# Kernel optimization log

Hardware: AMD Instinct MI355X
Metric: run time of the kernel (lower is better)

The kernel has to match this reference:

```python
import jax, jax.numpy as jnp
import numpy as np

TOP_K = 4
N_GROUP = 4
TOPK_GROUP = 2
ROUTED_SCALING = 1.0


def setup_inputs() -> dict:
    key = jax.random.key(0)
    k1, k2, k3, k4, k5 = jax.random.split(key, 5)
    B, S, H, I, E = 1, 2048, 1024, 512, 16
    hidden_states = jax.random.normal(k1, (B, S, H), dtype=jnp.float32)
    # router weight (kaiming-uniform-like scale)
    gate_weight = jax.random.normal(k2, (E, H), dtype=jnp.float32) * (1.0 / np.sqrt(H))
    e_bias = jnp.zeros((E,), dtype=jnp.float32)  # e_score_correction_bias buffer
    gate_proj = jax.random.normal(k3, (E, I, H), dtype=jnp.float32) * 0.02
    up_proj = jax.random.normal(k4, (E, I, H), dtype=jnp.float32) * 0.02
    down_proj = jax.random.normal(k5, (E, H, I), dtype=jnp.float32) * 0.02
    return {
        "hidden_states": hidden_states,
        "gate_weight": gate_weight,
        "e_bias": e_bias,
        "gate_proj": gate_proj,
        "up_proj": up_proj,
        "down_proj": down_proj,
    }


def _route(x_flat, gate_weight, e_bias):
    # x_flat: [T, H]
    T = x_flat.shape[0]
    E = gate_weight.shape[0]
    logits = jnp.einsum("th,eh->te", x_flat, gate_weight)
    scores = jax.nn.sigmoid(logits)                      # [T, E]
    scores_for_choice = scores + e_bias[None, :]
    # group scores = sum of top-2 expert scores within each group
    grp = scores_for_choice.reshape(T, N_GROUP, E // N_GROUP)
    top2, _ = jax.lax.top_k(grp, 2)
    group_scores = top2.sum(axis=-1)                     # [T, G]
    _, group_idx = jax.lax.top_k(group_scores, TOPK_GROUP)
    group_mask = jax.nn.one_hot(group_idx, N_GROUP, dtype=scores.dtype).sum(axis=1)  # [T, G]
    score_mask = jnp.repeat(group_mask, E // N_GROUP, axis=1)                        # [T, E]
    tmp_scores = jnp.where(score_mask > 0, scores_for_choice, 0.0)
    _, topk_idx = jax.lax.top_k(tmp_scores, TOP_K)       # [T, K]
    topk_weight = jnp.take_along_axis(scores, topk_idx, axis=1)
    denom = topk_weight.sum(axis=-1, keepdims=True) + 1e-20
    topk_weight = topk_weight / denom * ROUTED_SCALING
    return topk_idx, topk_weight


def reference(hidden_states, gate_weight, e_bias, gate_proj, up_proj, down_proj):
    B, S, H = hidden_states.shape
    E = gate_proj.shape[0]
    x = hidden_states.reshape(-1, H).astype(jnp.float32)  # [T, H]
    topk_idx, topk_weight = _route(x, gate_weight, e_bias)
    # combine weights per (token, expert): sum over the k slots selecting e
    combine = (jax.nn.one_hot(topk_idx, E, dtype=x.dtype) * topk_weight[..., None]).sum(axis=1)  # [T, E]
    # dense expert MLP (mathematically equal to gather-compute-scatter since
    # non-selected experts receive zero combine weight)
    g = jnp.einsum("th,eih->tei", x, gate_proj)
    u = jnp.einsum("th,eih->tei", x, up_proj)
    act = jax.nn.silu(g) * u                              # [T, E, I]
    expert_out = jnp.einsum("tei,ehi->teh", act, down_proj)
    y = jnp.einsum("teh,te->th", expert_out, combine)
    return y.reshape(B, S, H)
```

## Files before the change

kernel.cpp:

```cpp
#include <hip/hip_runtime.h>
#include <hip/hip_bf16.h>

typedef __attribute__((ext_vector_type(8))) short bf16x8;
typedef __attribute__((ext_vector_type(4))) float f32x4;

#define T_TOK 2048
#define HD 1024
#define ID 512
#define NE 16
#define TOPK 4
#define BK 32
#define WELEM (HD*ID*NE)
#define CPAD 16

__device__ __forceinline__ unsigned pk2(float a, float b) {
    return __builtin_amdgcn_perm(__float_as_uint(b), __float_as_uint(a),
                                 0x07060302u);
}
__device__ __forceinline__ bf16x8 cvt8(const float* __restrict__ p) {
    float4 a = *(const float4*)p;
    float4 b = *(const float4*)(p + 4);
    union { bf16x8 v; unsigned u[4]; } r;
    r.u[0] = pk2(a.x, a.y); r.u[1] = pk2(a.z, a.w);
    r.u[2] = pk2(b.x, b.y); r.u[3] = pk2(b.z, b.w);
    return r.v;
}
__device__ __forceinline__ short f2bf(float f) {
    unsigned u = __float_as_uint(f);
    return (short)((u + 0x7fffu + ((u >> 16) & 1u)) >> 16);
}
__device__ __forceinline__ float bf2f(short s) {
    return __uint_as_float(((unsigned)(unsigned short)s) << 16);
}
__device__ __forceinline__ void load_lds16(const short* g, short* l) {
    __builtin_amdgcn_global_load_lds(
        (const __attribute__((address_space(1))) unsigned*)g,
        (__attribute__((address_space(3))) unsigned*)l, 16, 0, 0);
}

#define MFMA_BF16 __builtin_amdgcn_mfma_f32_16x16x32_bf16

__global__ __launch_bounds__(256) void conv_k(
        const float* __restrict__ s0, short* __restrict__ d0,
        const float* __restrict__ s1, short* __restrict__ d1,
        const float* __restrict__ s2, short* __restrict__ d2,
        int* __restrict__ counts) {
    if (blockIdx.x == 0 && blockIdx.y == 0)
        counts[threadIdx.x] = 0;
    const float* src = (blockIdx.y == 0) ? s0 : (blockIdx.y == 1) ? s1 : s2;
    short* dst       = (blockIdx.y == 0) ? d0 : (blockIdx.y == 1) ? d1 : d2;
    size_t i = ((size_t)blockIdx.x * 256 + threadIdx.x) * 8;
    union { bf16x8 v; uint4 q; } r;
    r.v = cvt8(src + i);
    *(uint4*)(dst + i) = r.q;
}

__global__ __launch_bounds__(256) void router_k(
        const float* __restrict__ x, const float* __restrict__ gw,
        const float* __restrict__ eb,
        int* __restrict__ tk_idx, float* __restrict__ tk_w,
        short* __restrict__ xb,
        int* __restrict__ counts, int* __restrict__ tok_list,
        int* __restrict__ pair_slot) {
    int wid  = (blockIdx.x * 256 + threadIdx.x) >> 6;
    int lane = threadIdx.x & 63;

    const float* xr = x + (size_t)wid * HD + lane * 16;
    float xv[16];
#pragma unroll
    for (int c = 0; c < 4; c++) {
        float4 v = *(const float4*)(xr + c * 4);
        xv[4 * c] = v.x; xv[4 * c + 1] = v.y; xv[4 * c + 2] = v.z; xv[4 * c + 3] = v.w;
    }
    {
        union { uint4 q; unsigned u[4]; } w0, w1;
        w0.u[0] = pk2(xv[0], xv[1]);  w0.u[1] = pk2(xv[2], xv[3]);
        w0.u[2] = pk2(xv[4], xv[5]);  w0.u[3] = pk2(xv[6], xv[7]);
        w1.u[0] = pk2(xv[8], xv[9]);  w1.u[1] = pk2(xv[10], xv[11]);
        w1.u[2] = pk2(xv[12], xv[13]); w1.u[3] = pk2(xv[14], xv[15]);
        short* d = xb + ((size_t)wid << 10) + lane * 16;
        *(uint4*)d = w0.q;
        *(uint4*)(d + 8) = w1.q;
    }

    float logits[NE];
#pragma unroll
    for (int e = 0; e < NE; e++) {
        const float* gr = gw + e * HD + lane * 16;
        float p = 0.f;
#pragma unroll
        for (int c = 0; c < 4; c++) {
            float4 v = *(const float4*)(gr + c * 4);
            p += xv[4 * c] * v.x + xv[4 * c + 1] * v.y +
                 xv[4 * c + 2] * v.z + xv[4 * c + 3] * v.w;
        }
#pragma unroll
        for (int s = 32; s > 0; s >>= 1) p += __shfl_xor(p, s, 64);
        logits[e] = p;
    }

    float scores[NE], sc[NE];
#pragma unroll
    for (int e = 0; e < NE; e++) {
        scores[e] = 1.f / (1.f + __expf(-logits[e]));
        sc[e] = scores[e] + eb[e];
    }

    float gs[4];
#pragma unroll
    for (int g = 0; g < 4; g++) {
        float a = sc[4 * g], b = sc[4 * g + 1], c = sc[4 * g + 2], d = sc[4 * g + 3];
        float h1 = fmaxf(a, b), l1 = fminf(a, b);
        float h2 = fmaxf(c, d), l2 = fminf(c, d);
        gs[g] = fmaxf(h1, h2) + fmaxf(fminf(h1, h2), fmaxf(l1, l2));
    }
    int g0 = 0; float b0 = gs[0];
#pragma unroll
    for (int g = 1; g < 4; g++) if (gs[g] > b0) { b0 = gs[g]; g0 = g; }
    int g1 = -1; float b1 = -1e30f;
#pragma unroll
    for (int g = 0; g < 4; g++) if (g != g0 && gs[g] > b1) { b1 = gs[g]; g1 = g; }

    int taken = 0;
    int bid[TOPK]; float bsc[TOPK]; float wsum = 0.f;
#pragma unroll
    for (int k = 0; k < TOPK; k++) {
        float bv = -1e30f; int bi = 0; float bs = 0.f;
#pragma unroll
        for (int e = 0; e < NE; e++) {
            int grp = e >> 2;
            bool ok = ((grp == g0) || (grp == g1)) && !((taken >> e) & 1);
            if (ok && sc[e] > bv) { bv = sc[e]; bi = e; bs = scores[e]; }
        }
        taken |= (1 << bi);
        bid[k] = bi; bsc[k] = bs; wsum += bs;
    }
    if (lane < TOPK) {
        float inv = 1.0f / (wsum + 1e-20f);
        int ee = bid[lane];
        int slot = atomicAdd(&counts[ee * CPAD], 1);
        tok_list[ee * T_TOK + slot] = wid;
        pair_slot[wid * TOPK + lane] = slot;
        tk_idx[wid * TOPK + lane] = ee;
        tk_w[wid * TOPK + lane]   = bsc[lane] * inv;
    }
}

__global__ __launch_bounds__(256) void gemm1_k(
        const short* __restrict__ xb,
        const short* __restrict__ gpb,
        const short* __restrict__ upb,
        const int* __restrict__ counts,
        const int* __restrict__ tok_list,
        short* __restrict__ act) {
    __shared__ short xs[3][128 * BK];
    __shared__ short gs[3][64 * BK];
    __shared__ short us[3][64 * BK];
    __shared__ int   tok_s[128];

    int e = blockIdx.x;
    int cnt = counts[e * CPAD];
    int base = blockIdx.z * 128;
    if (base >= cnt) return;
    int off = 0;
#pragma unroll
    for (int q = 0; q < NE; q++) if (q < e) off += counts[q * CPAD];
    int arow0 = off + base;

    int tid = threadIdx.x;
    if (tid < 128) {
        int s = base + tid;
        tok_s[tid] = (s < cnt) ? tok_list[e * T_TOK + s] : tok_list[e * T_TOK];
    }
    __syncthreads();

    int wv = tid >> 6, lane = tid & 63;
    int qd = lane >> 4, l16 = lane & 15;
    int wm = (wv >> 1) * 64, wn = (wv & 1) * 32;
    int nb0 = blockIdx.y * 64;
    const short* gp = gpb + (size_t)e * ID * HD + (size_t)nb0 * HD;
    const short* up = upb + (size_t)e * ID * HD + (size_t)nb0 * HD;

    const short* xsg[2]; short* xld[2];
#pragma unroll
    for (int i = 0; i < 2; i++) {
        int idx = i * 256 + tid, r = idx >> 2, c = idx & 3;
        int f = (r >> 1) & 3;
        xsg[i] = xb + ((size_t)tok_s[r] << 10) + ((c ^ f) << 3);
        xld[i] = &xs[0][(i * 256 + wv * 64) * 8];
    }
    const short* gsg; const short* usg; short* gld; short* uld;
    {
        int r = tid >> 2, c = tid & 3;
        int f = (r >> 1) & 3;
        size_t so = (size_t)r * HD + ((c ^ f) << 3);
        gsg = gp + so;
        usg = up + so;
        gld = &gs[0][(wv * 64) * 8];
        uld = &us[0][(wv * 64) * 8];
    }

    f32x4 accg[4][2] = {};
    f32x4 accu[4][2] = {};

    auto STAGE = [&](int kp, int b) {
        load_lds16(xsg[0] + kp, xld[0] + b * (128 * BK));
        load_lds16(xsg[1] + kp, xld[1] + b * (128 * BK));
        load_lds16(gsg + kp, gld + b * (64 * BK));
        load_lds16(usg + kp, uld + b * (64 * BK));
    };
    auto COMPUTE = [&](int b) {
        const short* xsb = xs[b];
        const short* gsb = gs[b];
        const short* usb = us[b];
        bf16x8 af[4], bg[2], bu[2];
#pragma unroll
        for (int i = 0; i < 4; i++) {
            int r = wm + i * 16 + l16;
            af[i] = *(const bf16x8*)&xsb[r * BK + ((qd ^ ((r >> 1) & 3)) << 3)];
        }
#pragma unroll
        for (int j = 0; j < 2; j++) {
            int r = wn + j * 16 + l16;
            int lo = r * BK + ((qd ^ ((r >> 1) & 3)) << 3);
            bg[j] = *(const bf16x8*)&gsb[lo];
            bu[j] = *(const bf16x8*)&usb[lo];
        }
#pragma unroll
        for (int i = 0; i < 4; i++)
#pragma unroll
            for (int j = 0; j < 2; j++) {
                accg[i][j] = MFMA_BF16(af[i], bg[j], accg[i][j], 0, 0, 0);
                accu[i][j] = MFMA_BF16(af[i], bu[j], accu[i][j], 0, 0, 0);
            }
    };

    constexpr int NP = HD / BK;
    STAGE(0, 0); STAGE(BK, 1);
    int b = 0;
#pragma unroll 1
    for (int p = 0; p < NP; ++p) {
        int bn = b + 2; if (bn >= 3) bn -= 3;
        if (p + 2 < NP) {
            STAGE((p + 2) * BK, bn);
            asm volatile("s_waitcnt vmcnt(8)" ::: "memory");
        } else if (p + 1 < NP) {
            asm volatile("s_waitcnt vmcnt(4)" ::: "memory");
        } else {
            asm volatile("s_waitcnt vmcnt(0)" ::: "memory");
        }
        __builtin_amdgcn_s_barrier();
        asm volatile("" ::: "memory");
        COMPUTE(b);
        asm volatile("" ::: "memory");
        __builtin_amdgcn_s_barrier();
        b = (b == 2) ? 0 : b + 1;
    }

#pragma unroll
    for (int i = 0; i < 4; i++)
#pragma unroll
        for (int j = 0; j < 2; j++)
#pragma unroll
            for (int r = 0; r < 4; r++) {
                int m = wm + i * 16 + qd * 4 + r;
                if (base + m < cnt) {
                    float g = accg[i][j][r], u = accu[i][j][r];
                    float a = g / (1.f + __expf(-g)) * u;
                    act[(size_t)(arow0 + m) * ID + nb0 + wn + j * 16 + l16] = f2bf(a);
                }
            }
}

__global__ __launch_bounds__(256) void gemm2_k(
        const short* __restrict__ act,
        const short* __restrict__ dpb,
        const int* __restrict__ counts,
        short* __restrict__ yexp) {
    __shared__ short as_[3][128 * BK];
    __shared__ short ds_[3][128 * BK];

    int e = blockIdx.x;
    int cnt = counts[e * CPAD];
    int base = blockIdx.z * 128;
    if (base >= cnt) return;
    int off = 0;
#pragma unroll
    for (int q = 0; q < NE; q++) if (q < e) off += counts[q * CPAD];
    int arow0 = off + base;

    int tid = threadIdx.x;
    int wv = tid >> 6, lane = tid & 63;
    int qd = lane >> 4, l16 = lane & 15;
    int wm = (wv >> 1) * 64, wn = (wv & 1) * 64;
    int hb0 = blockIdx.y * 128;
    const short* dp = dpb + (size_t)e * HD * ID + (size_t)hb0 * ID;

    const short* asg[2]; const short* dsg[2]; short* ald[2]; short* dld[2];
#pragma unroll
    for (int i = 0; i < 2; i++) {
        int idx = i * 256 + tid, r = idx >> 2, c = idx & 3;
        int f = (r >> 1) & 3;
        int sw = (c ^ f) << 3;
        asg[i] = act + (size_t)(arow0 + r) * ID + sw;
        dsg[i] = dp + (size_t)r * ID + sw;
        ald[i] = &as_[0][(i * 256 + wv * 64) * 8];
        dld[i] = &ds_[0][(i * 256 + wv * 64) * 8];
    }

    f32x4 acc[4][4] = {};

    auto STAGE = [&](int kp, int b) {
        load_lds16(asg[0] + kp, ald[0] + b * (128 * BK));
        load_lds16(asg[1] + kp, ald[1] + b * (128 * BK));
        load_lds16(dsg[0] + kp, dld[0] + b * (128 * BK));
        load_lds16(dsg[1] + kp, dld[1] + b * (128 * BK));
    };
    auto COMPUTE = [&](int b) {
        const short* asb = as_[b];
        const short* dsb = ds_[b];
        bf16x8 af[4], bd[4];
#pragma unroll
        for (int i = 0; i < 4; i++) {
            int r = wm + i * 16 + l16;
            af[i] = *(const bf16x8*)&asb[r * BK + ((qd ^ ((r >> 1) & 3)) << 3)];
            int r2 = wn + i * 16 + l16;
            bd[i] = *(const bf16x8*)&dsb[r2 * BK + ((qd ^ ((r2 >> 1) & 3)) << 3)];
        }
#pragma unroll
        for (int i = 0; i < 4; i++)
#pragma unroll
            for (int j = 0; j < 4; j++)
                acc[i][j] = MFMA_BF16(af[i], bd[j], acc[i][j], 0, 0, 0);
    };

    constexpr int NP = ID / BK;
    STAGE(0, 0); STAGE(BK, 1);
    int b = 0;
#pragma unroll 1
    for (int p = 0; p < NP; ++p) {
        int bn = b + 2; if (bn >= 3) bn -= 3;
        if (p + 2 < NP) {
            STAGE((p + 2) * BK, bn);
            asm volatile("s_waitcnt vmcnt(8)" ::: "memory");
        } else if (p + 1 < NP) {
            asm volatile("s_waitcnt vmcnt(4)" ::: "memory");
        } else {
            asm volatile("s_waitcnt vmcnt(0)" ::: "memory");
        }
        __builtin_amdgcn_s_barrier();
        asm volatile("" ::: "memory");
        COMPUTE(b);
        asm volatile("" ::: "memory");
        __builtin_amdgcn_s_barrier();
        b = (b == 2) ? 0 : b + 1;
    }

#pragma unroll
    for (int i = 0; i < 4; i++)
#pragma unroll
        for (int j = 0; j < 4; j++)
#pragma unroll
            for (int r = 0; r < 4; r++) {
                int m = wm + i * 16 + qd * 4 + r;
                if (base + m < cnt)
                    yexp[(size_t)(arow0 + m) * HD + hb0 + wn + j * 16 + l16] =
                        f2bf(acc[i][j][r]);
            }
}

__global__ __launch_bounds__(256) void combine_k(
        const short* __restrict__ yexp,
        const int* __restrict__ counts,
        const int* __restrict__ tk_idx, const float* __restrict__ tk_w,
        const int* __restrict__ pair_slot,
        float* __restrict__ out) {
    __shared__ int offs_s[NE];
    if (threadIdx.x == 0) {
        int a = 0;
#pragma unroll
        for (int e = 0; e < NE; e++) { offs_s[e] = a; a += counts[e * CPAD]; }
    }
    __syncthreads();

    int t = blockIdx.x * 2 + (threadIdx.x >> 7);
    int i = threadIdx.x & 127;
    float acc[8] = {};
#pragma unroll
    for (int k = 0; k < TOPK; k++) {
        int p = t * TOPK + k;
        int e = tk_idx[p];
        int row = offs_s[e] + pair_slot[p];
        float w = tk_w[p];
        bf16x8 v = *(const bf16x8*)(yexp + (size_t)row * HD + i * 8);
#pragma unroll
        for (int j = 0; j < 8; j++) acc[j] += w * bf2f(v[j]);
    }
    float4 o0 = {acc[0], acc[1], acc[2], acc[3]};
    float4 o1 = {acc[4], acc[5], acc[6], acc[7]};
    float* d = out + (size_t)t * HD + i * 8;
    *(float4*)d = o0;
    *(float4*)(d + 4) = o1;
}

extern "C" void kernel_launch(void* const* d_in, const int* in_sizes, int n_in,
                              void* d_out, int out_size, void* d_ws, size_t ws_size,
                              hipStream_t stream) {
    const float* x  = (const float*)d_in[0];
    const float* gw = (const float*)d_in[1];
    const float* eb = (const float*)d_in[2];
    const float* gp = (const float*)d_in[3];
    const float* up = (const float*)d_in[4];
    const float* dp = (const float*)d_in[5];

    short* gpb = (short*)d_ws;
    short* upb = gpb + WELEM;
    short* dpb = upb + WELEM;
    short* xb  = dpb + WELEM;
    short* act = xb + (size_t)T_TOK * HD;
    int* counts    = (int*)(act + (size_t)(T_TOK * TOPK + 128) * ID);
    int* tok_list  = counts + NE * CPAD;
    int* pair_slot = tok_list + NE * T_TOK;
    int* tk_idx    = pair_slot + T_TOK * TOPK;
    float* tk_w    = (float*)(tk_idx + T_TOK * TOPK);
    short* yexp = gpb;

    conv_k<<<dim3(WELEM / 8 / 256, 3), 256, 0, stream>>>(gp, gpb, up, upb,
                                                         dp, dpb, counts);
    router_k<<<T_TOK / 4, 256, 0, stream>>>(x, gw, eb, tk_idx, tk_w, xb,
                                            counts, tok_list, pair_slot);
    gemm1_k<<<dim3(NE, ID / 64, T_TOK / 128), 256, 0, stream>>>(
        xb, gpb, upb, counts, tok_list, act);
    gemm2_k<<<dim3(NE, HD / 128, T_TOK / 128), 256, 0, stream>>>(
        act, dpb, counts, yexp);
    combine_k<<<T_TOK / 2, 256, 0, stream>>>(yexp, counts, tk_idx, tk_w,
                                             pair_slot, (float*)d_out);
}
```

Baseline: 214.3 us.

## Fuse fp32-to-bf16 weight conversion into expert GEMM tile loads

Removes the standalone conversion kernel that turned all three expert weight tensors into bf16 in workspace. The GEMM kernels now read fp32 weights straight into registers, pack them to bf16 and store them to a single LDS buffer, prefetching one step ahead in registers. Token and activation tiles keep the async global-to-LDS triple buffer. This cuts a full pass over the weights plus the bf16 write-back, but every token tile of an expert now re-reads fp32 weights (twice the bytes), and the single B buffer needs an extra barrier per step.

```diff
diff --git a/kernel.cpp b/kernel.cpp
--- a/kernel.cpp
+++ b/kernel.cpp
@@ -10,20 +10,11 @@
 #define NE 16
 #define TOPK 4
 #define BK 32
-#define WELEM (HD*ID*NE)
 #define CPAD 16
 
 __device__ __forceinline__ unsigned pk2(float a, float b) {
     return __builtin_amdgcn_perm(__float_as_uint(b), __float_as_uint(a),
                                  0x07060302u);
-}
-__device__ __forceinline__ bf16x8 cvt8(const float* __restrict__ p) {
-    float4 a = *(const float4*)p;
-    float4 b = *(const float4*)(p + 4);
-    union { bf16x8 v; unsigned u[4]; } r;
-    r.u[0] = pk2(a.x, a.y); r.u[1] = pk2(a.z, a.w);
-    r.u[2] = pk2(b.x, b.y); r.u[3] = pk2(b.z, b.w);
-    return r.v;
 }
 __device__ __forceinline__ short f2bf(float f) {
     unsigned u = __float_as_uint(f);
@@ -39,21 +30,7 @@
 }
 
 #define MFMA_BF16 __builtin_amdgcn_mfma_f32_16x16x32_bf16
-
-__global__ __launch_bounds__(256) void conv_k(
-        const float* __restrict__ s0, short* __restrict__ d0,
-        const float* __restrict__ s1, short* __restrict__ d1,
-        const float* __restrict__ s2, short* __restrict__ d2,
-        int* __restrict__ counts) {
-    if (blockIdx.x == 0 && blockIdx.y == 0)
-        counts[threadIdx.x] = 0;
-    const float* src = (blockIdx.y == 0) ? s0 : (blockIdx.y == 1) ? s1 : s2;
-    short* dst       = (blockIdx.y == 0) ? d0 : (blockIdx.y == 1) ? d1 : d2;
-    size_t i = ((size_t)blockIdx.x * 256 + threadIdx.x) * 8;
-    union { bf16x8 v; uint4 q; } r;
-    r.v = cvt8(src + i);
-    *(uint4*)(dst + i) = r.q;
-}
+#define FENCE() asm volatile("" ::: "memory")
 
 __global__ __launch_bounds__(256) void router_k(
         const float* __restrict__ x, const float* __restrict__ gw,
@@ -148,14 +125,14 @@
 
 __global__ __launch_bounds__(256) void gemm1_k(
         const short* __restrict__ xb,
-        const short* __restrict__ gpb,
-        const short* __restrict__ upb,
+        const float* __restrict__ gpf,
+        const float* __restrict__ upf,
         const int* __restrict__ counts,
         const int* __restrict__ tok_list,
         short* __restrict__ act) {
     __shared__ short xs[3][128 * BK];
-    __shared__ short gs[3][64 * BK];
-    __shared__ short us[3][64 * BK];
+    __shared__ short gsm[64 * BK];
+    __shared__ short usm[64 * BK];
     __shared__ int   tok_s[128];
 
     int e = blockIdx.x;
@@ -178,8 +155,6 @@
     int qd = lane >> 4, l16 = lane & 15;
     int wm = (wv >> 1) * 64, wn = (wv & 1) * 32;
     int nb0 = blockIdx.y * 64;
-    const short* gp = gpb + (size_t)e * ID * HD + (size_t)nb0 * HD;
-    const short* up = upb + (size_t)e * ID * HD + (size_t)nb0 * HD;
 
     const short* xsg[2]; short* xld[2];
 #pragma unroll
@@ -189,30 +164,39 @@
         xsg[i] = xb + ((size_t)tok_s[r] << 10) + ((c ^ f) << 3);
         xld[i] = &xs[0][(i * 256 + wv * 64) * 8];
     }
-    const short* gsg; const short* usg; short* gld; short* uld;
-    {
-        int r = tid >> 2, c = tid & 3;
-        int f = (r >> 1) & 3;
-        size_t so = (size_t)r * HD + ((c ^ f) << 3);
-        gsg = gp + so;
-        usg = up + so;
-        gld = &gs[0][(wv * 64) * 8];
-        uld = &us[0][(wv * 64) * 8];
-    }
+    int br = tid >> 2, bc = tid & 3;
+    int bf_ = (br >> 1) & 3;
+    const float* gsrc = gpf + (size_t)e * ID * HD + (size_t)(nb0 + br) * HD + bc * 8;
+    const float* usrc = upf + (size_t)e * ID * HD + (size_t)(nb0 + br) * HD + bc * 8;
+    short* gdst = &gsm[br * BK + ((bc ^ bf_) << 3)];
+    short* udst = &usm[br * BK + ((bc ^ bf_) << 3)];
 
     f32x4 accg[4][2] = {};
     f32x4 accu[4][2] = {};
-
-    auto STAGE = [&](int kp, int b) {
+    float4 gA0, gA1, uA0, uA1, gB0, gB1, uB0, uB1;
+
+    auto XDMA = [&](int kp, int b) {
         load_lds16(xsg[0] + kp, xld[0] + b * (128 * BK));
         load_lds16(xsg[1] + kp, xld[1] + b * (128 * BK));
-        load_lds16(gsg + kp, gld + b * (64 * BK));
-        load_lds16(usg + kp, uld + b * (64 * BK));
+    };
+    auto BLOAD = [&](int kp, float4& g0, float4& g1, float4& u0, float4& u1) {
+        g0 = *(const float4*)(gsrc + kp);
+        g1 = *(const float4*)(gsrc + kp + 4);
+        u0 = *(const float4*)(usrc + kp);
+        u1 = *(const float4*)(usrc + kp + 4);
+    };
+    auto BWRITE = [&](const float4& g0, const float4& g1,
+                      const float4& u0, const float4& u1) {
+        uint4 t;
+        t.x = pk2(g0.x, g0.y); t.y = pk2(g0.z, g0.w);
+        t.z = pk2(g1.x, g1.y); t.w = pk2(g1.z, g1.w);
+        *(uint4*)gdst = t;
+        t.x = pk2(u0.x, u0.y); t.y = pk2(u0.z, u0.w);
+        t.z = pk2(u1.x, u1.y); t.w = pk2(u1.z, u1.w);
+        *(uint4*)udst = t;
     };
     auto COMPUTE = [&](int b) {
         const short* xsb = xs[b];
-        const short* gsb = gs[b];
-        const short* usb = us[b];
         bf16x8 af[4], bg[2], bu[2];
 #pragma unroll
         for (int i = 0; i < 4; i++) {
@@ -223,8 +207,8 @@
         for (int j = 0; j < 2; j++) {
             int r = wn + j * 16 + l16;
             int lo = r * BK + ((qd ^ ((r >> 1) & 3)) << 3);
-            bg[j] = *(const bf16x8*)&gsb[lo];
-            bu[j] = *(const bf16x8*)&usb[lo];
+            bg[j] = *(const bf16x8*)&gsm[lo];
+            bu[j] = *(const bf16x8*)&usm[lo];
         }
 #pragma unroll
         for (int i = 0; i < 4; i++)
@@ -236,26 +220,53 @@
     };
 
     constexpr int NP = HD / BK;
-    STAGE(0, 0); STAGE(BK, 1);
-    int b = 0;
+    BLOAD(0, gA0, gA1, uA0, uA1);
+    FENCE();
+    XDMA(0, 0); XDMA(BK, 1);
+    FENCE();
 #pragma unroll 1
-    for (int p = 0; p < NP; ++p) {
-        int bn = b + 2; if (bn >= 3) bn -= 3;
-        if (p + 2 < NP) {
-            STAGE((p + 2) * BK, bn);
-            asm volatile("s_waitcnt vmcnt(8)" ::: "memory");
-        } else if (p + 1 < NP) {
-            asm volatile("s_waitcnt vmcnt(4)" ::: "memory");
-        } else {
-            asm volatile("s_waitcnt vmcnt(0)" ::: "memory");
-        }
-        __builtin_amdgcn_s_barrier();
-        asm volatile("" ::: "memory");
-        COMPUTE(b);
-        asm volatile("" ::: "memory");
-        __builtin_amdgcn_s_barrier();
-        b = (b == 2) ? 0 : b + 1;
-    }
+    for (int p = 0; p < NP - 2; p += 2) {
+        BLOAD((p + 1) * BK, gB0, gB1, uB0, uB1);
+        FENCE();
+        XDMA((p + 2) * BK, (p + 2) % 3);
+        FENCE();
+        asm volatile("s_waitcnt vmcnt(8)" ::: "memory");
+        BWRITE(gA0, gA1, uA0, uA1);
+        asm volatile("s_waitcnt lgkmcnt(0)" ::: "memory");
+        __builtin_amdgcn_s_barrier();
+        FENCE();
+        COMPUTE(p % 3);
+        FENCE();
+        __builtin_amdgcn_s_barrier();
+        BLOAD((p + 2) * BK, gA0, gA1, uA0, uA1);
+        FENCE();
+        XDMA((p + 3) * BK, (p + 3) % 3);
+        FENCE();
+        asm volatile("s_waitcnt vmcnt(8)" ::: "memory");
+        BWRITE(gB0, gB1, uB0, uB1);
+        asm volatile("s_waitcnt lgkmcnt(0)" ::: "memory");
+        __builtin_amdgcn_s_barrier();
+        FENCE();
+        COMPUTE((p + 1) % 3);
+        FENCE();
+        __builtin_amdgcn_s_barrier();
+    }
+    BLOAD((NP - 1) * BK, gB0, gB1, uB0, uB1);
+    FENCE();
+    asm volatile("s_waitcnt vmcnt(6)" ::: "memory");
+    BWRITE(gA0, gA1, uA0, uA1);
+    asm volatile("s_waitcnt lgkmcnt(0)" ::: "memory");
+    __builtin_amdgcn_s_barrier();
+    FENCE();
+    COMPUTE((NP - 2) % 3);
+    FENCE();
+    __builtin_amdgcn_s_barrier();
+    asm volatile("s_waitcnt vmcnt(0)" ::: "memory");
+    BWRITE(gB0, gB1, uB0, uB1);
+    asm volatile("s_waitcnt lgkmcnt(0)" ::: "memory");
+    __builtin_amdgcn_s_barrier();
+    FENCE();
+    COMPUTE((NP - 1) % 3);
 
 #pragma unroll
     for (int i = 0; i < 4; i++)
@@ -274,11 +285,11 @@
 
 __global__ __launch_bounds__(256) void gemm2_k(
         const short* __restrict__ act,
-        const short* __restrict__ dpb,
+        const float* __restrict__ dpf,
         const int* __restrict__ counts,
         short* __restrict__ yexp) {
     __shared__ short as_[3][128 * BK];
-    __shared__ short ds_[3][128 * BK];
+    __shared__ short dsm[128 * BK];
 
     int e = blockIdx.x;
     int cnt = counts[e * CPAD];
@@ -294,38 +305,59 @@
     int qd = lane >> 4, l16 = lane & 15;
     int wm = (wv >> 1) * 64, wn = (wv & 1) * 64;
     int hb0 = blockIdx.y * 128;
-    const short* dp = dpb + (size_t)e * HD * ID + (size_t)hb0 * ID;
-
-    const short* asg[2]; const short* dsg[2]; short* ald[2]; short* dld[2];
+
+    const short* asg[2]; short* ald[2];
 #pragma unroll
     for (int i = 0; i < 2; i++) {
         int idx = i * 256 + tid, r = idx >> 2, c = idx & 3;
         int f = (r >> 1) & 3;
-        int sw = (c ^ f) << 3;
-        asg[i] = act + (size_t)(arow0 + r) * ID + sw;
-        dsg[i] = dp + (size_t)r * ID + sw;
+        asg[i] = act + (size_t)(arow0 + r) * ID + ((c ^ f) << 3);
         ald[i] = &as_[0][(i * 256 + wv * 64) * 8];
-        dld[i] = &ds_[0][(i * 256 + wv * 64) * 8];
+    }
+    const float* dsrc0; const float* dsrc1; short* ddst0; short* ddst1;
+    {
+        int idx = tid, r = idx >> 2, c = idx & 3;
+        int f = (r >> 1) & 3;
+        dsrc0 = dpf + (size_t)e * HD * ID + (size_t)(hb0 + r) * ID + c * 8;
+        ddst0 = &dsm[r * BK + ((c ^ f) << 3)];
+        idx = 256 + tid; r = idx >> 2; c = idx & 3;
+        f = (r >> 1) & 3;
+        dsrc1 = dpf + (size_t)e * HD * ID + (size_t)(hb0 + r) * ID + c * 8;
+        ddst1 = &dsm[r * BK + ((c ^ f) << 3)];
     }
 
     f32x4 acc[4][4] = {};
-
-    auto STAGE = [&](int kp, int b) {
+    float4 dA0, dA1, dA2, dA3, dB0, dB1, dB2, dB3;
+
+    auto XDMA = [&](int kp, int b) {
         load_lds16(asg[0] + kp, ald[0] + b * (128 * BK));
         load_lds16(asg[1] + kp, ald[1] + b * (128 * BK));
-        load_lds16(dsg[0] + kp, dld[0] + b * (128 * BK));
-        load_lds16(dsg[1] + kp, dld[1] + b * (128 * BK));
+    };
+    auto BLOAD = [&](int kp, float4& d0, float4& d1, float4& d2, float4& d3) {
+        d0 = *(const float4*)(dsrc0 + kp);
+        d1 = *(const float4*)(dsrc0 + kp + 4);
+        d2 = *(const float4*)(dsrc1 + kp);
+        d3 = *(const float4*)(dsrc1 + kp + 4);
+    };
+    auto BWRITE = [&](const float4& d0, const float4& d1,
+                      const float4& d2, const float4& d3) {
+        uint4 t;
+        t.x = pk2(d0.x, d0.y); t.y = pk2(d0.z, d0.w);
+        t.z = pk2(d1.x, d1.y); t.w = pk2(d1.z, d1.w);
+        *(uint4*)ddst0 = t;
+        t.x = pk2(d2.x, d2.y); t.y = pk2(d2.z, d2.w);
+        t.z = pk2(d3.x, d3.y); t.w = pk2(d3.z, d3.w);
+        *(uint4*)ddst1 = t;
     };
     auto COMPUTE = [&](int b) {
         const short* asb = as_[b];
-        const short* dsb = ds_[b];
         bf16x8 af[4], bd[4];
 #pragma unroll
         for (int i = 0; i < 4; i++) {
             int r = wm + i * 16 + l16;
             af[i] = *(const bf16x8*)&asb[r * BK + ((qd ^ ((r >> 1) & 3)) << 3)];
             int r2 = wn + i * 16 + l16;
-            bd[i] = *(const bf16x8*)&dsb[r2 * BK + ((qd ^ ((r2 >> 1) & 3)) << 3)];
+            bd[i] = *(const bf16x8*)&dsm[r2 * BK + ((qd ^ ((r2 >> 1) & 3)) << 3)];
         }
 #pragma unroll
         for (int i = 0; i < 4; i++)
@@ -335,26 +367,53 @@
     };
 
     constexpr int NP = ID / BK;
-    STAGE(0, 0); STAGE(BK, 1);
-    int b = 0;
+    BLOAD(0, dA0, dA1, dA2, dA3);
+    FENCE();
+    XDMA(0, 0); XDMA(BK, 1);
+    FENCE();
 #pragma unroll 1
-    for (int p = 0; p < NP; ++p) {
-        int bn = b + 2; if (bn >= 3) bn -= 3;
-        if (p + 2 < NP) {
-            STAGE((p + 2) * BK, bn);
-            asm volatile("s_waitcnt vmcnt(8)" ::: "memory");
-        } else if (p + 1 < NP) {
-            asm volatile("s_waitcnt vmcnt(4)" ::: "memory");
-        } else {
-            asm volatile("s_waitcnt vmcnt(0)" ::: "memory");
-        }
-        __builtin_amdgcn_s_barrier();
-        asm volatile("" ::: "memory");
-        COMPUTE(b);
-        asm volatile("" ::: "memory");
-        __builtin_amdgcn_s_barrier();
-        b = (b == 2) ? 0 : b + 1;
-    }
+    for (int p = 0; p < NP - 2; p += 2) {
+        BLOAD((p + 1) * BK, dB0, dB1, dB2, dB3);
+        FENCE();
+        XDMA((p + 2) * BK, (p + 2) % 3);
+        FENCE();
+        asm volatile("s_waitcnt vmcnt(8)" ::: "memory");
+        BWRITE(dA0, dA1, dA2, dA3);
+        asm volatile("s_waitcnt lgkmcnt(0)" ::: "memory");
+        __builtin_amdgcn_s_barrier();
+        FENCE();
+        COMPUTE(p % 3);
+        FENCE();
+        __builtin_amdgcn_s_barrier();
+        BLOAD((p + 2) * BK, dA0, dA1, dA2, dA3);
+        FENCE();
+        XDMA((p + 3) * BK, (p + 3) % 3);
+        FENCE();
+        asm volatile("s_waitcnt vmcnt(8)" ::: "memory");
+        BWRITE(dB0, dB1, dB2, dB3);
+        asm volatile("s_waitcnt lgkmcnt(0)" ::: "memory");
+        __builtin_amdgcn_s_barrier();
+        FENCE();
+        COMPUTE((p + 1) % 3);
+        FENCE();
+        __builtin_amdgcn_s_barrier();
+    }
+    BLOAD((NP - 1) * BK, dB0, dB1, dB2, dB3);
+    FENCE();
+    asm volatile("s_waitcnt vmcnt(6)" ::: "memory");
+    BWRITE(dA0, dA1, dA2, dA3);
+    asm volatile("s_waitcnt lgkmcnt(0)" ::: "memory");
+    __builtin_amdgcn_s_barrier();
+    FENCE();
+    COMPUTE((NP - 2) % 3);
+    FENCE();
+    __builtin_amdgcn_s_barrier();
+    asm volatile("s_waitcnt vmcnt(0)" ::: "memory");
+    BWRITE(dB0, dB1, dB2, dB3);
+    asm volatile("s_waitcnt lgkmcnt(0)" ::: "memory");
+    __builtin_amdgcn_s_barrier();
+    FENCE();
+    COMPUTE((NP - 1) % 3);
 
 #pragma unroll
     for (int i = 0; i < 4; i++)
@@ -413,26 +472,23 @@
     const float* up = (const float*)d_in[4];
     const float* dp = (const float*)d_in[5];
 
-    short* gpb = (short*)d_ws;
-    short* upb = gpb + WELEM;
-    short* dpb = upb + WELEM;
-    short* xb  = dpb + WELEM;
-    short* act = xb + (size_t)T_TOK * HD;
-    int* counts    = (int*)(act + (size_t)(T_TOK * TOPK + 128) * ID);
+    short* xb   = (short*)d_ws;
+    short* act  = xb + (size_t)T_TOK * HD;
+    short* yexp = act + (size_t)(T_TOK * TOPK + 128) * ID;
+    int* counts    = (int*)(yexp + (size_t)T_TOK * TOPK * HD);
     int* tok_list  = counts + NE * CPAD;
     int* pair_slot = tok_list + NE * T_TOK;
     int* tk_idx    = pair_slot + T_TOK * TOPK;
     float* tk_w    = (float*)(tk_idx + T_TOK * TOPK);
-    short* yexp = gpb;
-
-    conv_k<<<dim3(WELEM / 8 / 256, 3), 256, 0, stream>>>(gp, gpb, up, upb,
-                                                         dp, dpb, counts);
+
+    hipMemsetAsync(counts, 0, NE * CPAD * sizeof(int), stream);
+
     router_k<<<T_TOK / 4, 256, 0, stream>>>(x, gw, eb, tk_idx, tk_w, xb,
                                             counts, tok_list, pair_slot);
     gemm1_k<<<dim3(NE, ID / 64, T_TOK / 128), 256, 0, stream>>>(
-        xb, gpb, upb, counts, tok_list, act);
+        xb, gp, up, counts, tok_list, act);
     gemm2_k<<<dim3(NE, HD / 128, T_TOK / 128), 256, 0, stream>>>(
-        act, dpb, counts, yexp);
+        act, dp, counts, yexp);
     combine_k<<<T_TOK / 2, 256, 0, stream>>>(yexp, counts, tk_idx, tk_w,
                                              pair_slot, (float*)d_out);
 }
```

After: 242.2 us. 13.0% more time.
